# Kernel optimization log

Hardware: AMD Instinct MI355X
Metric: run time of the kernel (lower is better)

The kernel has to match this reference:

```python
import jax, jax.numpy as jnp
import numpy as np

# Config matching init_kwargs: dim=256, input_resolution=(64,64), num_heads=8,
# stride=2, dynamic_factor=2, window_size=8, Attention_Group=2, postype='rel', k=None
DIM, H, W = 256, 64, 64
HEADS, HG, STRIDE, WS, FACTOR = 8, 2, 2, 8, 2.0
GC = DIM // HG                 # channels per attention group (offset net width)
HC = DIM // HEADS              # per-head channels
RH, RW = H // STRIDE, W // STRIDE
WH, WW = H // WS, W // WS
B = 2
MLP_HID = 4 * DIM
EPS = 1e-5


def _grid_sample(img, grid):
    # img: (N, C, H, W); grid: (N, Hg, Wg, 2) with (row, col) in [-1, 1].
    # Bilinear, align_corners=True, zero padding (matches F.grid_sample).
    N, C, Hi, Wi = img.shape
    rows = (grid[..., 0] + 1.0) * 0.5 * (Hi - 1)
    cols = (grid[..., 1] + 1.0) * 0.5 * (Wi - 1)
    r0f = jnp.floor(rows); c0f = jnp.floor(cols)
    wr = rows - r0f; wc = cols - c0f
    r0 = r0f.astype(jnp.int32); c0 = c0f.astype(jnp.int32)

    def gather(ri, ci):
        valid = ((ri >= 0) & (ri < Hi) & (ci >= 0) & (ci < Wi)).astype(img.dtype)
        rc = jnp.clip(ri, 0, Hi - 1); cc = jnp.clip(ci, 0, Wi - 1)
        vals = jax.vmap(lambda im, r, c: im[:, r, c])(img, rc, cc)  # (N, C, Hg, Wg)
        return vals * valid[:, None]

    return (gather(r0, c0) * ((1 - wr) * (1 - wc))[:, None]
            + gather(r0, c0 + 1) * ((1 - wr) * wc)[:, None]
            + gather(r0 + 1, c0) * (wr * (1 - wc))[:, None]
            + gather(r0 + 1, c0 + 1) * (wr * wc)[:, None])


def _ln2d(z, g, b):
    mu = jnp.mean(z, axis=1, keepdims=True)
    var = jnp.var(z, axis=1, keepdims=True)
    return (z - mu) * jax.lax.rsqrt(var + EPS) * g[None, :, None, None] + b[None, :, None, None]


def _conv1x1(z, w, b=None):
    out = jnp.einsum('oc,bchw->bohw', w, z)
    return out if b is None else out + b[None, :, None, None]


def _forward(x, ln1_g, ln1_b, q_w, q_b, k_w, k_b, v_w, v_b,
             off1_w, off2_w, off3_w, bn_g, bn_b, bn_m, bn_v, off4_w,
             posembed, proj_w, proj_b, ln2_g, ln2_b,
             mlp_w1, mlp_b1, mlp_w2, mlp_b2):
    Bx, C = x.shape[0], x.shape[1]
    R, NW, WT = RH * RW, WH * WW, WS * WS
    scale = C ** -0.5  # original uses dim**-0.5 (not head_dim) as default qk scale

    xa = _ln2d(x, ln1_g, ln1_b)
    q = _conv1x1(xa, q_w, q_b)

    # ---- per-group offset prediction: 3 depthwise strided convs -> BN -> GELU -> 1x1 ----
    qg = q.reshape(Bx * HG, GC, H, W)

    def dw(z, w):
        return jax.lax.conv_general_dilated(z, w, (2, 2), ((1, 1), (1, 1)),
                feature_group_count=GC, dimension_numbers=('NCHW', 'OIHW', 'NCHW'))

    o = dw(dw(dw(qg, off1_w), off2_w), off3_w)  # (B*HG, GC, WH, WW)
    o = (o - bn_m[None, :, None, None]) * jax.lax.rsqrt(bn_v + EPS)[None, :, None, None]
    o = o * bn_g[None, :, None, None] + bn_b[None, :, None, None]
    o = jax.nn.gelu(o, approximate=False)
    off = jnp.einsum('oc,bchw->bohw', off4_w, o)               # (B*HG, 2R, WH, WW)
    off = off.reshape(Bx * HG, 2, R, NW).transpose(0, 3, 2, 1)  # (B*HG, NW, R, 2)
    ranges = jnp.array([1.0 / H, 1.0 / W], dtype=x.dtype)
    off = jnp.tanh(off) * ranges * FACTOR

    # ---- reference points normalized to [-1, 1] (align_corners=True convention) ----
    ref_r = (jnp.arange(RH, dtype=x.dtype) * STRIDE) / (H - 1) * 2.0 - 1.0
    ref_c = (jnp.arange(RW, dtype=x.dtype) * STRIDE) / (W - 1) * 2.0 - 1.0
    ref = jnp.stack(jnp.meshgrid(ref_r, ref_c, indexing='ij'), axis=-1).reshape(R, 2)
    grid = off + ref[None, None]                                # (B*HG, NW, R, 2)

    # ---- deformable gather of values at predicted sample locations ----
    value = xa.reshape(Bx * HG, GC, H, W)
    samp = _grid_sample(value, grid).reshape(Bx, C, NW, R)

    kk = _conv1x1(samp, k_w, k_b).reshape(Bx * HEADS, HC, NW, R).transpose(0, 2, 1, 3)
    vv = _conv1x1(samp, v_w, v_b).reshape(Bx * HEADS, HC, NW, R).transpose(0, 2, 1, 3)

    # ---- windowed queries ----
    wq = q.reshape(Bx * HEADS, HC, H, W).transpose(0, 2, 3, 1)
    wq = wq.reshape(Bx * HEADS, WH, WS, WW, WS, HC).transpose(0, 1, 3, 2, 4, 5)
    wq = wq.reshape(Bx * HEADS, NW, WT, HC) * scale

    attn = jnp.einsum('nwqc,nwcr->nwqr', wq, kk)                # (B*h, NW, WT, R)

    # ---- relative position bias: query pixel vs. (stride-spaced) reference point ----
    rel_y = (jnp.arange(RH) * STRIDE)[None, :] - jnp.arange(H)[:, None] + (H - 1)  # (H, RH)
    rel_x = (jnp.arange(RW) * STRIDE)[None, :] - jnp.arange(W)[:, None] + (W - 1)  # (W, RW)
    t = posembed[:, rel_y, :]                                   # (h, H, RH, 2W-1)
    bias = t[:, :, :, rel_x]                                    # (h, H, RH, W, RW)
    bias = bias.transpose(0, 1, 3, 2, 4).reshape(HEADS, H, W, R)
    bias = bias.reshape(HEADS, WH, WS, WW, WS, R).transpose(0, 1, 3, 2, 4, 5)
    bias = bias.reshape(HEADS, NW, WT, R)

    attn = attn.reshape(Bx, HEADS, NW, WT, R) + bias[None]
    attn = jax.nn.softmax(attn, axis=-1).reshape(Bx * HEADS, NW, WT, R)
    out = jnp.einsum('nwqr,nwcr->nwqc', attn, vv)               # (B*h, NW, WT, HC)
    out = out.reshape(Bx * HEADS, WH, WW, WS, WS, HC).transpose(0, 1, 3, 2, 4, 5)
    out = out.reshape(Bx, HEADS, H, W, HC).transpose(0, 1, 4, 2, 3).reshape(Bx, C, H, W)
    out = _conv1x1(out, proj_w, proj_b)

    x = x + out
    xm = _ln2d(x, ln2_g, ln2_b)
    hdn = jax.nn.gelu(_conv1x1(xm, mlp_w1, mlp_b1), approximate=False)
    return x + _conv1x1(hdn, mlp_w2, mlp_b2)


def setup_inputs() -> dict:
    key = jax.random.key(0)
    ks = jax.random.split(key, 16)
    f32 = jnp.float32

    def n(k, shape, std=0.02):
        return jax.random.normal(k, shape, dtype=f32) * std

    R = RH * RW
    return {
        'x': jax.random.normal(ks[0], (B, DIM, H, W), dtype=f32),
        'ln1_g': jnp.ones((DIM,), f32), 'ln1_b': jnp.zeros((DIM,), f32),
        'q_w': n(ks[1], (DIM, DIM)), 'q_b': jnp.zeros((DIM,), f32),
        'k_w': n(ks[2], (DIM, DIM)), 'k_b': jnp.zeros((DIM,), f32),
        'v_w': n(ks[3], (DIM, DIM)), 'v_b': jnp.zeros((DIM,), f32),
        'off1_w': n(ks[4], (GC, 1, 3, 3)),
        'off2_w': n(ks[5], (GC, 1, 3, 3)),
        'off3_w': n(ks[6], (GC, 1, 3, 3)),
        'bn_g': jnp.ones((GC,), f32), 'bn_b': jnp.zeros((GC,), f32),
        'bn_m': jnp.zeros((GC,), f32), 'bn_v': jnp.ones((GC,), f32),
        'off4_w': n(ks[7], (2 * R, GC)),
        'posembed': n(ks[8], (HEADS, 2 * H - 1, 2 * W - 1), std=0.01),
        'proj_w': n(ks[9], (DIM, DIM)), 'proj_b': jnp.zeros((DIM,), f32),
        'ln2_g': jnp.ones((DIM,), f32), 'ln2_b': jnp.zeros((DIM,), f32),
        'mlp_w1': n(ks[10], (MLP_HID, DIM)), 'mlp_b1': jnp.zeros((MLP_HID,), f32),
        'mlp_w2': n(ks[11], (DIM, MLP_HID)), 'mlp_b2': jnp.zeros((DIM,), f32),
    }


def reference(x, ln1_g, ln1_b, q_w, q_b, k_w, k_b, v_w, v_b,
              off1_w, off2_w, off3_w, bn_g, bn_b, bn_m, bn_v, off4_w,
              posembed, proj_w, proj_b, ln2_g, ln2_b,
              mlp_w1, mlp_b1, mlp_w2, mlp_b2):
    return _forward(x, ln1_g, ln1_b, q_w, q_b, k_w, k_b, v_w, v_b,
                    off1_w, off2_w, off3_w, bn_g, bn_b, bn_m, bn_v, off4_w,
                    posembed, proj_w, proj_b, ln2_g, ln2_b,
                    mlp_w1, mlp_b1, mlp_w2, mlp_b2)
```

## Files before the change

kernel.cpp:

```cpp
#include <hip/hip_runtime.h>
#include <hip/hip_bf16.h>
#include <math.h>


typedef __hip_bfloat16 bf16;
typedef __bf16 bf16x8 __attribute__((ext_vector_type(8)));
typedef float f32x4 __attribute__((ext_vector_type(4)));
typedef unsigned int u32x4 __attribute__((ext_vector_type(4)));

union U16x8 { uint4 u4; u32x4 v4; unsigned short us[8]; };
union FU { float f; unsigned int u; };

__device__ __forceinline__ float cvt(float x) { return x; }
__device__ __forceinline__ float cvt(bf16 x) { return __bfloat162float(x); }
__device__ __forceinline__ float b2f(unsigned short u) {
  union { float f; unsigned int v; } x; x.v = ((unsigned int)u) << 16; return x.f;
}
__device__ __forceinline__ float hi2f(unsigned int u) {
  FU x; x.u = u & 0xffff0000u; return x.f;
}
__device__ __forceinline__ float lo2f(unsigned int u) {
  FU x; x.u = u << 16; return x.f;
}
__device__ __forceinline__ unsigned short f2b(float f) {
  bf16 h = __float2bfloat16(f);
  return *reinterpret_cast<unsigned short*>(&h);
}
__device__ __forceinline__ float gelu_f(float x) {
  return 0.5f * x * (1.0f + erff(x * 0.7071067811865475f));
}
__device__ __forceinline__ void stout(float* p, float v) { *p = v; }
__device__ __forceinline__ void stout(bf16* p, float v) { *p = __float2bfloat16(v); }

__global__ __launch_bounds__(256) void setup_kernel(
    const float* __restrict__ x, const float* __restrict__ g,
    const float* __restrict__ bta,
    const float* __restrict__ q_w, const float* __restrict__ q_b,
    const float* __restrict__ k_w, const float* __restrict__ v_w,
    const float* __restrict__ pjw, const float* __restrict__ w1,
    const float* __restrict__ w2, const float* __restrict__ off4w,
    bf16* __restrict__ out, float* __restrict__ xnhwc,
    unsigned short* __restrict__ wqkv, float* __restrict__ bqkv,
    unsigned short* __restrict__ wproj, unsigned short* __restrict__ wmlp1,
    unsigned short* __restrict__ wmlp2, unsigned short* __restrict__ woff4i)
{
  __shared__ float s1[8][32], s2[8][32];
  __shared__ unsigned short tb[32][264];
  int bid = blockIdx.x;
  int t = threadIdx.x;
  if (bid < 256) {
    int pos = t & 31, cs = t >> 5;
    int p = bid * 32 + pos;
    int bb = p >> 12, hw = p & 4095;
    const float* xp = x + (size_t)bb * 256 * 4096 + hw;
    float vloc[32];
    float sum = 0.f, ss = 0.f;
#pragma unroll
    for (int i = 0; i < 32; ++i) {
      float v = xp[(size_t)(cs * 32 + i) * 4096];
      vloc[i] = v; sum += v; ss += v * v;
    }
    s1[cs][pos] = sum; s2[cs][pos] = ss;
    {
      float* xo = xnhwc + (size_t)p * 256 + cs * 32;
#pragma unroll
      for (int qd = 0; qd < 8; ++qd)
        *(float4*)(xo + qd * 4) = make_float4(vloc[qd*4], vloc[qd*4+1],
                                              vloc[qd*4+2], vloc[qd*4+3]);
    }
    __syncthreads();
    if (cs == 0) {
      float S = 0.f, Q = 0.f;
#pragma unroll
      for (int i = 0; i < 8; ++i) { S += s1[i][pos]; Q += s2[i][pos]; }
      float mu = S * (1.f / 256.f);
      float var = Q * (1.f / 256.f) - mu * mu;
      s1[0][pos] = mu;
      s2[0][pos] = rsqrtf(var + 1e-5f);
    }
    __syncthreads();
    float mu = s1[0][pos], rs = s2[0][pos];
#pragma unroll
    for (int i = 0; i < 32; ++i) {
      int c = cs * 32 + i;
      tb[pos][c] = f2b((vloc[i] - mu) * rs * g[c] + bta[c]);
    }
    __syncthreads();
    int px = t >> 3, grp = t & 7;
    bf16* op = out + ((size_t)bid * 32 + px) * 256 + grp * 32;
#pragma unroll
    for (int q = 0; q < 4; ++q)
      *(uint4*)(op + q * 8) = *(const uint4*)&tb[px][grp * 32 + q * 8];
  } else {
    int idx = (bid - 256) * 256 + t;
    const int S0 = 768 * 256;
    const int S1 = S0 + 768;
    const int S2 = S1 + 256 * 256;
    const int S3 = S2 + 1024 * 256;
    const int S4 = S3 + 256 * 1024;
    const int S5 = S4 + 2048 * 128;
    if (idx < S0) {
      int n = idx >> 8, c = idx & 255;
      float v;
      if (n < 256)       v = q_w[n * 256 + c];
      else if (n < 512)  v = k_w[(n - 256) * 256 + c];
      else               v = v_w[(n - 512) * 256 + c];
      wqkv[idx] = f2b(v);
    } else if (idx < S1) {
      int n = idx - S0;
      bqkv[n] = (n < 256) ? q_b[n] : 0.f;
    } else if (idx < S2) {
      wproj[idx - S1] = f2b(pjw[idx - S1]);
    } else if (idx < S3) {
      wmlp1[idx - S2] = f2b(w1[idx - S2]);
    } else if (idx < S4) {
      wmlp2[idx - S3] = f2b(w2[idx - S3]);
    } else if (idx < S5) {
      int kk = idx - S4;
      int n = kk >> 7, c = kk & 127;
      woff4i[kk] = f2b(off4w[((size_t)((n & 1) * 1024 + (n >> 1))) * 128 + c]);
    }
  }
}

__global__ __launch_bounds__(256) void ln2_kernel(
    const bf16* __restrict__ xin, const float* __restrict__ g,
    const float* __restrict__ bta, bf16* __restrict__ out)
{
  __shared__ float sa[8][32], sb[8][32];
  __shared__ float mu_s[32], rs_s[32];
  int t = threadIdx.x;
  int px = t >> 3, grp = t & 7;
  size_t p = (size_t)blockIdx.x * 32 + px;
  const bf16* xp = xin + p * 256 + grp * 32;
  float v[32]; float sum = 0.f, ss = 0.f;
#pragma unroll
  for (int q = 0; q < 4; ++q) {
    U16x8 u; u.u4 = *(const uint4*)(xp + q * 8);
#pragma unroll
    for (int j = 0; j < 8; ++j) {
      float f = b2f(u.us[j]); v[q * 8 + j] = f; sum += f; ss += f * f;
    }
  }
  sa[grp][px] = sum; sb[grp][px] = ss;
  __syncthreads();
  if (t < 32) {
    float S = 0.f, Q = 0.f;
#pragma unroll
    for (int i = 0; i < 8; ++i) { S += sa[i][t]; Q += sb[i][t]; }
    float mu = S * (1.f / 256.f);
    mu_s[t] = mu;
    rs_s[t] = rsqrtf(Q * (1.f / 256.f) - mu * mu + 1e-5f);
  }
  __syncthreads();
  float mu = mu_s[px], rs = rs_s[px];
  bf16* op = out + p * 256 + grp * 32;
#pragma unroll
  for (int q = 0; q < 4; ++q) {
    U16x8 o;
#pragma unroll
    for (int j = 0; j < 8; ++j) {
      int c = grp * 32 + q * 8 + j;
      o.us[j] = f2b((v[q * 8 + j] - mu) * rs * g[c] + bta[c]);
    }
    *(uint4*)(op + q * 8) = o.u4;
  }
}

template<int OUTM, int RESM, int ACT, int BM, int BN>
__global__ __launch_bounds__(256) void mgemm_kernel(
    const bf16* __restrict__ A, const unsigned short* __restrict__ Bw,
    const float* __restrict__ bias, const void* __restrict__ res,
    void* __restrict__ out, int N, int K, int lda, int ldb)
{
  constexpr int MT = BM / 32;
  constexpr int WNT = BN / 32;
  constexpr int AB_BYTES = (BM + BN) * 72 * 2;
  constexpr int T_LD = BM + 5;
  constexpr int T_BYTES = 64 * T_LD * 4;
  constexpr int SH_BYTES = (OUTM == 1 && T_BYTES > AB_BYTES) ? T_BYTES : AB_BYTES;
  __shared__ __attribute__((aligned(16))) char shraw[SH_BYTES];
  auto As = reinterpret_cast<unsigned short(*)[72]>(shraw);
  auto Bs = reinterpret_cast<unsigned short(*)[72]>(shraw + BM * 72 * 2);
  float (*T)[T_LD] = reinterpret_cast<float(*)[T_LD]>(shraw);

  int t = threadIdx.x;
  int m0 = blockIdx.y * BM, n0 = blockIdx.x * BN;
  int lane = t & 63, w = t >> 6;
  int l15 = lane & 15, quad = lane >> 4;
  int wm = (w >> 1) * (BM / 2), wn = (w & 1) * (BN / 2);
  f32x4 acc[MT][WNT];
#pragma unroll
  for (int mt = 0; mt < MT; ++mt)
#pragma unroll
    for (int nt = 0; nt < WNT; ++nt) acc[mt][nt] = (f32x4){0.f, 0.f, 0.f, 0.f};

  for (int k0 = 0; k0 < K; k0 += 64) {
#pragma unroll
    for (int i = 0; i < MT; ++i) {
      int idx = t + i * 256;
      int m = idx >> 3, oc = (idx & 7) * 8;
      *(uint4*)&As[m][oc] = *(const uint4*)(A + (size_t)(m0 + m) * lda + k0 + oc);
    }
#pragma unroll
    for (int i = 0; i < WNT; ++i) {
      int idx = t + i * 256;
      int n = idx >> 3, oc = (idx & 7) * 8;
      *(uint4*)&Bs[n][oc] = *(const uint4*)(Bw + (size_t)(n0 + n) * ldb + k0 + oc);
    }
    __syncthreads();
#pragma unroll
    for (int ks = 0; ks < 2; ++ks) {
      bf16x8 af[MT], bfr[WNT];
#pragma unroll
      for (int mt = 0; mt < MT; ++mt)
        af[mt] = __builtin_bit_cast(bf16x8,
            *(const uint4*)&As[wm + mt * 16 + l15][ks * 32 + quad * 8]);
#pragma unroll
      for (int nt = 0; nt < WNT; ++nt)
        bfr[nt] = __builtin_bit_cast(bf16x8,
            *(const uint4*)&Bs[wn + nt * 16 + l15][ks * 32 + quad * 8]);
#pragma unroll
      for (int mt = 0; mt < MT; ++mt)
#pragma unroll
        for (int nt = 0; nt < WNT; ++nt)
          acc[mt][nt] = __builtin_amdgcn_mfma_f32_16x16x32_bf16(
              af[mt], bfr[nt], acc[mt][nt], 0, 0, 0);
    }
    __syncthreads();
  }
  float bv[WNT];
#pragma unroll
  for (int nt = 0; nt < WNT; ++nt)
    bv[nt] = bias ? bias[n0 + wn + nt * 16 + l15] : 0.f;
#pragma unroll
  for (int mt = 0; mt < MT; ++mt) {
#pragma unroll
    for (int nt = 0; nt < WNT; ++nt) {
#pragma unroll
      for (int reg = 0; reg < 4; ++reg) {
        int m = m0 + wm + mt * 16 + quad * 4 + reg;
        int n = n0 + wn + nt * 16 + l15;
        float v = acc[mt][nt][reg] + bv[nt];
        if constexpr (ACT == 1) v = gelu_f(v);
        if constexpr (RESM == 1)
          v += ((const float*)res)[(size_t)m * N + n];
        if constexpr (RESM == 2)
          v += b2f(((const unsigned short*)res)[(size_t)m * N + n]);
        if constexpr (OUTM == 0)
          ((unsigned short*)out)[(size_t)m * N + n] = f2b(v);
        if constexpr (OUTM == 1)
          T[(n - n0)][(m - m0)] = v;
        if constexpr (OUTM == 4)
          ((unsigned short*)out)[((size_t)(n >> 8) * 8192 + m) * 256 + (n & 255)] = f2b(v);
        if constexpr (OUTM == 5) {
          float val = tanhf(v) * (2.0f / 64.0f);
          int r = n >> 1, coord = n & 1;
          int rc = coord ? (r & 31) : (r >> 5);
          float ref = rc * (4.0f / 63.0f) - 1.0f;
          float pix = (val + ref + 1.0f) * 31.5f;
          float other = __shfl_xor(pix, 1, 64);
          if (coord == 0) {
            float rowp = pix, colp = other;
            float r0f = floorf(rowp), c0f = floorf(colp);
            float wr = rowp - r0f, wc = colp - c0f;
            int r0 = (int)r0f, c0 = (int)c0f;
            bool rv0 = ((unsigned)r0 < 64u), rv1 = ((unsigned)(r0 + 1) < 64u);
            bool cv0 = ((unsigned)c0 < 64u), cv1 = ((unsigned)(c0 + 1) < 64u);
            float4 w4;
            w4.x = (rv0 && cv0) ? (1.f - wr) * (1.f - wc) : 0.f;
            w4.y = (rv0 && cv1) ? (1.f - wr) * wc : 0.f;
            w4.z = (rv1 && cv0) ? wr * (1.f - wc) : 0.f;
            w4.w = (rv1 && cv1) ? wr * wc : 0.f;
            ((int*)out)[(size_t)m * 1024 + r] = r0 * 64 + c0;
            *(float4*)((float*)res + ((size_t)m * 1024 + r) * 4) = w4;
          }
        }
      }
    }
  }
  if constexpr (OUTM == 1) {
    __syncthreads();
    constexpr int SEGS = BM / 32;
    int units = 64 * SEGS;
    if (t < units) {
      int nl = t / SEGS, seg = t % SEGS;
      int bI = m0 >> 12, hw0 = m0 & 4095;
      float* op = (float*)out + ((size_t)bI * 256 + n0 + nl) * 4096 + hw0 + seg * 32;
#pragma unroll
      for (int k = 0; k < 32; ++k) op[k] = T[nl][seg * 32 + k];
    }
  }
}

template<typename TI, typename TO, int IC>
__global__ __launch_bounds__(256) void dwconv_kernel(
    const TI* __restrict__ in, const float* __restrict__ wgt,
    TO* __restrict__ out, int Hi, int Wi, int Ho, int Wo, int fuse,
    const float* __restrict__ bg_, const float* __restrict__ bb_,
    const float* __restrict__ bm_, const float* __restrict__ bv_)
{
  int idx = blockIdx.x * 256 + threadIdx.x;
  int c = idx & 127;
  int pp = idx >> 7;
  int ow = pp % Wo, oh = (pp / Wo) % Ho, bgi = pp / (Wo * Ho);
  const TI* ip;
  if constexpr (IC == 256)
    ip = in + ((size_t)(bgi >> 1) * 4096) * 256 + (bgi & 1) * 128 + c;
  else
    ip = in + ((size_t)bgi * Hi * Wi) * 128 + c;
  float acc = 0.f;
#pragma unroll
  for (int ky = 0; ky < 3; ++ky) {
    int ih = oh * 2 - 1 + ky;
    if ((unsigned)ih >= (unsigned)Hi) continue;
#pragma unroll
    for (int kx = 0; kx < 3; ++kx) {
      int iw = ow * 2 - 1 + kx;
      if ((unsigned)iw >= (unsigned)Wi) continue;
      acc += wgt[c * 9 + ky * 3 + kx] * cvt(ip[(size_t)(ih * Wi + iw) * IC]);
    }
  }
  if (fuse) {
    acc = (acc - bm_[c]) * rsqrtf(bv_[c] + 1e-5f) * bg_[c] + bb_[c];
    acc = gelu_f(acc);
  }
  stout(out + idx, acc);
}

__global__ __launch_bounds__(256) void gatherkv_kernel(
    const unsigned short* __restrict__ Kimg, const unsigned short* __restrict__ Vimg,
    const int* __restrict__ goff, const float* __restrict__ gwt,
    unsigned short* __restrict__ Ks, unsigned short* __restrict__ Vs)
{
  int t = threadIdx.x;
  int pos = blockIdx.x * 8 + (t >> 5);
  int oct = t & 31;
  int r = pos & 1023;
  int nw = (pos >> 10) & 63;
  int b = pos >> 16;
  int ch0 = oct * 8;
  int g = oct >> 4;

  size_t cbase = ((size_t)(b * 2 + g) * 64 + nw) * 1024 + r;
  int base = goff[cbase];
  f32x4 wv = *(const f32x4*)(gwt + cbase * 4);
  int o00 = min(max(base, 0), 4095);
  int o01 = min(max(base + 1, 0), 4095);
  int o10 = min(max(base + 64, 0), 4095);
  int o11 = min(max(base + 65, 0), 4095);
  size_t pb = ((size_t)b * 4096) * 256 + ch0;
  uint4 kc[4], vc[4];
  kc[0] = *(const uint4*)(Kimg + pb + (size_t)o00 * 256);
  kc[1] = *(const uint4*)(Kimg + pb + (size_t)o01 * 256);
  kc[2] = *(const uint4*)(Kimg + pb + (size_t)o10 * 256);
  kc[3] = *(const uint4*)(Kimg + pb + (size_t)o11 * 256);
  vc[0] = *(const uint4*)(Vimg + pb + (size_t)o00 * 256);
  vc[1] = *(const uint4*)(Vimg + pb + (size_t)o01 * 256);
  vc[2] = *(const uint4*)(Vimg + pb + (size_t)o10 * 256);
  vc[3] = *(const uint4*)(Vimg + pb + (size_t)o11 * 256);

  float aK[8] = {0.f,0.f,0.f,0.f,0.f,0.f,0.f,0.f};
  float aV[8] = {0.f,0.f,0.f,0.f,0.f,0.f,0.f,0.f};
#pragma unroll
  for (int c4 = 0; c4 < 4; ++c4) {
    U16x8 ku, vu; ku.u4 = kc[c4]; vu.u4 = vc[c4];
    float wvv = wv[c4];
#pragma unroll
    for (int j = 0; j < 8; ++j) {
      aK[j] += wvv * b2f(ku.us[j]);
      aV[j] += wvv * b2f(vu.us[j]);
    }
  }
  U16x8 ok, ov;
#pragma unroll
  for (int j = 0; j < 8; ++j) { ok.us[j] = f2b(aK[j]); ov.us[j] = f2b(aV[j]); }
  int head = oct >> 2, chh = (oct & 3) * 8;
  size_t obase = (((size_t)(b * 8 + head) * 64 + nw) * 1024 + r) * 32 + chh;
  __builtin_nontemporal_store(ok.v4, (u32x4*)(Ks + obase));
  __builtin_nontemporal_store(ov.v4, (u32x4*)(Vs + obase));
}

__global__ __launch_bounds__(256) void attn2_kernel(
    const bf16* __restrict__ qbuf, const unsigned short* __restrict__ Ks,
    const unsigned short* __restrict__ Vs, const float* __restrict__ vbv,
    const float* __restrict__ pe, bf16* __restrict__ aout)
{
  __shared__ unsigned short vs[2][32][72];
  __shared__ unsigned short PsQs[64][72];
  __shared__ unsigned short pesb[70][72];

  const float LOG2E = 1.4426950408889634f;
  int blk = blockIdx.x;
  int b = blk & 1, head = (blk >> 1) & 7, nw = blk >> 4;
  int wh = nw >> 3, ww = nw & 7;
  int t = threadIdx.x;
  int lane = t & 63, w = t >> 6;
  int l15 = lane & 15, quad = lane >> 4;
  int qc0 = head * 32;
  int vr = t >> 2, vseg = t & 3;

  size_t kvbase = ((size_t)(b * 8 + head) * 64 + nw) * 32768;
  const unsigned short* Kb = Ks + kvbase;
  const unsigned short* Vb = Vs + kvbase;

  {
    int qt = t >> 2, oct = t & 3;
    int h = wh * 8 + (qt >> 3), wcol = ww * 8 + (qt & 7);
    const bf16* src = qbuf + ((size_t)b * 4096 + h * 64 + wcol) * 256 + qc0 + oct * 8;
    U16x8 u; u.u4 = *(const uint4*)src;
    U16x8 o;
#pragma unroll
    for (int j = 0; j < 8; ++j) o.us[j] = f2b(b2f(u.us[j]) * (0.0625f * LOG2E));
    *(uint4*)&PsQs[qt][oct * 8] = o.u4;
  }
  int ry0 = 56 - wh * 8, rx0 = 56 - ww * 8;
  for (int i = t; i < 70 * 70; i += 256) {
    int yy = i / 70, xx = i % 70;
    pesb[yy][xx] = f2b(pe[(size_t)head * 16129 + (ry0 + yy) * 127 + rx0 + xx] * LOG2E);
  }
  {
    U16x8 vu; vu.u4 = *(const uint4*)(Vb + (size_t)t * 8);
#pragma unroll
    for (int j = 0; j < 8; ++j) {
      int row = vseg * 8 + j;
      vs[0][row][vr ^ (((row >> 3) & 3) * 8)] = vu.us[j];
    }
  }
  uint4 kf[4];
#pragma unroll
  for (int nt = 0; nt < 4; ++nt)
    kf[nt] = *(const uint4*)(Kb + (size_t)(nt * 16 + l15) * 32 + quad * 8);
  __syncthreads();

  bf16x8 aQ = __builtin_bit_cast(bf16x8, *(const uint4*)&PsQs[w * 16 + l15][quad * 8]);
  float l[4] = {0.f, 0.f, 0.f, 0.f};
  f32x4 oacc[2];
  oacc[0] = (f32x4){0.f, 0.f, 0.f, 0.f};
  oacc[1] = (f32x4){0.f, 0.f, 0.f, 0.f};

  int rowbase = 7 - (w * 2 + (quad >> 1));
  int Cb = 2 * l15 + 7 - (quad & 1) * 4;

  uint4 vcn = make_uint4(0u, 0u, 0u, 0u);
  uint4 kfn[4];
  for (int c = 0; c < 16; ++c) {
    int cur = c & 1;
    if (c) {
      U16x8 vu; vu.u4 = vcn;
#pragma unroll
      for (int j = 0; j < 8; ++j) {
        int row = vseg * 8 + j;
        vs[cur][row][vr ^ (((row >> 3) & 3) * 8)] = vu.us[j];
      }
      __syncthreads();
    }
    if (c < 15) {
      size_t nb = (size_t)(c * 64 + 64) * 32;
      vcn = *(const uint4*)(Vb + nb + (size_t)t * 8);
#pragma unroll
      for (int nt = 0; nt < 4; ++nt)
        kfn[nt] = *(const uint4*)(Kb + nb + (size_t)(nt * 16 + l15) * 32 + quad * 8);
    }

    f32x4 s[4];
    __builtin_amdgcn_s_setprio(1);
#pragma unroll
    for (int nt = 0; nt < 4; ++nt) {
      bf16x8 bK = __builtin_bit_cast(bf16x8, kf[nt]);
      f32x4 z = (f32x4){0.f, 0.f, 0.f, 0.f};
      s[nt] = __builtin_amdgcn_mfma_f32_16x16x32_bf16(aQ, bK, z, 0, 0, 0);
    }
    __builtin_amdgcn_s_setprio(0);
#pragma unroll
    for (int nt = 0; nt < 4; ++nt) {
      int row = rowbase + 4 * c + 2 * (nt >> 1);
      int C = Cb + (nt & 1) * 32;
      const unsigned int* pr = (const unsigned int*)&pesb[row][0];
      unsigned int pa = pr[(C - 3) >> 1];
      unsigned int pbm = pr[(C - 1) >> 1];
      s[nt][0] += hi2f(pbm);
      s[nt][1] += lo2f(pbm);
      s[nt][2] += hi2f(pa);
      s[nt][3] += lo2f(pa);
    }
#pragma unroll
    for (int reg = 0; reg < 4; ++reg) {
      float ps = 0.f;
#pragma unroll
      for (int nt = 0; nt < 4; ++nt) {
        float p = exp2f(s[nt][reg]);
        PsQs[w * 16 + quad * 4 + reg][nt * 16 + l15] = f2b(p);
        ps += p;
      }
      l[reg] += ps;
    }
    __builtin_amdgcn_s_setprio(1);
#pragma unroll
    for (int kst = 0; kst < 2; ++kst) {
      uint4 up = *(const uint4*)&PsQs[w * 16 + l15][kst * 32 + quad * 8];
      bf16x8 pA = __builtin_bit_cast(bf16x8, up);
#pragma unroll
      for (int nt2 = 0; nt2 < 2; ++nt2) {
        int row = nt2 * 16 + l15;
        int cbase = (kst * 32 + quad * 8) ^ (((row >> 3) & 3) * 8);
        uint4 uv = *(const uint4*)&vs[cur][row][cbase];
        bf16x8 vB = __builtin_bit_cast(bf16x8, uv);
        oacc[nt2] = __builtin_amdgcn_mfma_f32_16x16x32_bf16(pA, vB, oacc[nt2], 0, 0, 0);
      }
    }
    __builtin_amdgcn_s_setprio(0);
    if (c < 15) {
#pragma unroll
      for (int nt = 0; nt < 4; ++nt) kf[nt] = kfn[nt];
    }
  }
#pragma unroll
  for (int reg = 0; reg < 4; ++reg) {
    l[reg] += __shfl_xor(l[reg], 1, 64);
    l[reg] += __shfl_xor(l[reg], 2, 64);
    l[reg] += __shfl_xor(l[reg], 4, 64);
    l[reg] += __shfl_xor(l[reg], 8, 64);
  }
#pragma unroll
  for (int nt2 = 0; nt2 < 2; ++nt2) {
    float vbias = vbv[qc0 + nt2 * 16 + l15];
#pragma unroll
    for (int reg = 0; reg < 4; ++reg) {
      int q = w * 16 + quad * 4 + reg;
      size_t p = (size_t)b * 4096 + (wh * 8 + (q >> 3)) * 64 + ww * 8 + (q & 7);
      aout[p * 256 + qc0 + nt2 * 16 + l15] =
          __float2bfloat16(oacc[nt2][reg] / l[reg] + vbias);
    }
  }
}

extern "C" void kernel_launch(void* const* d_in, const int* in_sizes, int n_in,
                              void* d_out, int out_size, void* d_ws, size_t ws_size,
                              hipStream_t stream) {
  (void)in_sizes; (void)n_in; (void)out_size; (void)ws_size;
  const float* x     = (const float*)d_in[0];
  const float* ln1g  = (const float*)d_in[1];
  const float* ln1b  = (const float*)d_in[2];
  const float* q_w   = (const float*)d_in[3];
  const float* q_b   = (const float*)d_in[4];
  const float* k_w   = (const float*)d_in[5];
  const float* k_b   = (const float*)d_in[6];
  const float* v_w   = (const float*)d_in[7];
  const float* v_b   = (const float*)d_in[8];
  const float* off1w = (const float*)d_in[9];
  const float* off2w = (const float*)d_in[10];
  const float* off3w = (const float*)d_in[11];
  const float* bng   = (const float*)d_in[12];
  const float* bnb   = (const float*)d_in[13];
  const float* bnm   = (const float*)d_in[14];
  const float* bnv   = (const float*)d_in[15];
  const float* off4w = (const float*)d_in[16];
  const float* pe    = (const float*)d_in[17];
  const float* pjw   = (const float*)d_in[18];
  const float* pjb   = (const float*)d_in[19];
  const float* ln2g  = (const float*)d_in[20];
  const float* ln2b  = (const float*)d_in[21];
  const float* w1    = (const float*)d_in[22];
  const float* b1    = (const float*)d_in[23];
  const float* w2    = (const float*)d_in[24];
  const float* b2    = (const float*)d_in[25];
  (void)k_b;
  float* outp = (float*)d_out;

  char* W = (char*)d_ws;
  bf16*  xa    = (bf16*) (W + 0);
  float* dw1   = (float*)(W + 8388608);
  float* dw2   = (float*)(W + 10485760);
  bf16*  dw3b  = (bf16*) (W + 11010048);
  bf16*  qkv   = (bf16*) (W + 13238272);
  bf16*  qb    = qkv;
  bf16*  Kimg  = qkv + 2097152;
  bf16*  Vimg  = qkv + 2 * 2097152;
  bf16*  x2    = (bf16*) (W + 34209792);
  float* xnhwc = (float*)(W + 38404096);
  unsigned short* wqkv   = (unsigned short*)(W + 46792704);
  float*          bqkv   = (float*)         (W + 47448064);
  unsigned short* wproj  = (unsigned short*)(W + 47453184);
  unsigned short* wmlp1  = (unsigned short*)(W + 47584256);
  unsigned short* wmlp2  = (unsigned short*)(W + 48108544);
  unsigned short* woff4i = (unsigned short*)(W + 48632832);
  int*   goff  = (int*)  (W + 49157120);
  float* gwt   = (float*)(W + 50205696);
  unsigned short* Ksmp = (unsigned short*)(W + 54525952);
  unsigned short* Vsmp = (unsigned short*)(W + 121634816);
  bf16*  aout = xa;
  bf16*  xm   = xa;
  bf16*  hdn  = Kimg;

  setup_kernel<<<4356, 256, 0, stream>>>(
      x, ln1g, ln1b, q_w, q_b, k_w, v_w, pjw, w1, w2, off4w,
      xa, xnhwc, wqkv, bqkv, wproj, wmlp1, wmlp2, woff4i);
  mgemm_kernel<4, 0, 0, 128, 128><<<dim3(6, 64), 256, 0, stream>>>(
      xa, wqkv, bqkv, nullptr, qkv, 768, 256, 256, 256);
  dwconv_kernel<bf16, float, 256><<<2048, 256, 0, stream>>>(
      qb, off1w, dw1, 64, 64, 32, 32, 0, nullptr, nullptr, nullptr, nullptr);
  dwconv_kernel<float, float, 128><<<512, 256, 0, stream>>>(
      dw1, off2w, dw2, 32, 32, 16, 16, 0, nullptr, nullptr, nullptr, nullptr);
  dwconv_kernel<float, bf16, 128><<<128, 256, 0, stream>>>(
      dw2, off3w, dw3b, 16, 16, 8, 8, 1, bng, bnb, bnm, bnv);
  mgemm_kernel<5, 0, 0, 64, 64><<<dim3(32, 4), 256, 0, stream>>>(
      dw3b, woff4i, nullptr, (const void*)gwt, goff, 2048, 128, 128, 128);
  gatherkv_kernel<<<16384, 256, 0, stream>>>(
      (const unsigned short*)Kimg, (const unsigned short*)Vimg,
      goff, gwt, Ksmp, Vsmp);
  attn2_kernel<<<1024, 256, 0, stream>>>(
      qb, Ksmp, Vsmp, v_b, pe, aout);
  mgemm_kernel<0, 1, 0, 64, 128><<<dim3(2, 128), 256, 0, stream>>>(
      aout, wproj, pjb, (const void*)xnhwc, x2, 256, 256, 256, 256);
  ln2_kernel<<<256, 256, 0, stream>>>(x2, ln2g, ln2b, xm);
  mgemm_kernel<0, 0, 1, 128, 128><<<dim3(8, 64), 256, 0, stream>>>(
      xm, wmlp1, b1, nullptr, hdn, 1024, 256, 256, 256);
  mgemm_kernel<1, 2, 0, 64, 64><<<dim3(4, 128), 256, 0, stream>>>(
      hdn, wmlp2, b2, (const void*)x2, outp, 256, 1024, 1024, 1024);
}
```

Baseline: 278.9 us.

## Fuse bilinear K/V gather into attention kernel and retune GEMM tiles

Removes the separate gather kernel that wrote sampled K/V to large global buffers. The attention kernel now gathers and bilinearly combines K/V for each 64-key chunk directly into double-buffered shared memory, overlapping the next chunk's loads with the current chunk's MFMAs. This eliminates a large global write and re-read of intermediate K/V. The price is more per-block load latency and register pressure in attention. The tile widths of several GEMM launches are also halved to get more blocks.

```diff
diff --git a/kernel.cpp b/kernel.cpp
--- a/kernel.cpp
+++ b/kernel.cpp
@@ -328,64 +328,13 @@
   stout(out + idx, acc);
 }
 
-__global__ __launch_bounds__(256) void gatherkv_kernel(
-    const unsigned short* __restrict__ Kimg, const unsigned short* __restrict__ Vimg,
-    const int* __restrict__ goff, const float* __restrict__ gwt,
-    unsigned short* __restrict__ Ks, unsigned short* __restrict__ Vs)
-{
-  int t = threadIdx.x;
-  int pos = blockIdx.x * 8 + (t >> 5);
-  int oct = t & 31;
-  int r = pos & 1023;
-  int nw = (pos >> 10) & 63;
-  int b = pos >> 16;
-  int ch0 = oct * 8;
-  int g = oct >> 4;
-
-  size_t cbase = ((size_t)(b * 2 + g) * 64 + nw) * 1024 + r;
-  int base = goff[cbase];
-  f32x4 wv = *(const f32x4*)(gwt + cbase * 4);
-  int o00 = min(max(base, 0), 4095);
-  int o01 = min(max(base + 1, 0), 4095);
-  int o10 = min(max(base + 64, 0), 4095);
-  int o11 = min(max(base + 65, 0), 4095);
-  size_t pb = ((size_t)b * 4096) * 256 + ch0;
-  uint4 kc[4], vc[4];
-  kc[0] = *(const uint4*)(Kimg + pb + (size_t)o00 * 256);
-  kc[1] = *(const uint4*)(Kimg + pb + (size_t)o01 * 256);
-  kc[2] = *(const uint4*)(Kimg + pb + (size_t)o10 * 256);
-  kc[3] = *(const uint4*)(Kimg + pb + (size_t)o11 * 256);
-  vc[0] = *(const uint4*)(Vimg + pb + (size_t)o00 * 256);
-  vc[1] = *(const uint4*)(Vimg + pb + (size_t)o01 * 256);
-  vc[2] = *(const uint4*)(Vimg + pb + (size_t)o10 * 256);
-  vc[3] = *(const uint4*)(Vimg + pb + (size_t)o11 * 256);
-
-  float aK[8] = {0.f,0.f,0.f,0.f,0.f,0.f,0.f,0.f};
-  float aV[8] = {0.f,0.f,0.f,0.f,0.f,0.f,0.f,0.f};
-#pragma unroll
-  for (int c4 = 0; c4 < 4; ++c4) {
-    U16x8 ku, vu; ku.u4 = kc[c4]; vu.u4 = vc[c4];
-    float wvv = wv[c4];
-#pragma unroll
-    for (int j = 0; j < 8; ++j) {
-      aK[j] += wvv * b2f(ku.us[j]);
-      aV[j] += wvv * b2f(vu.us[j]);
-    }
-  }
-  U16x8 ok, ov;
-#pragma unroll
-  for (int j = 0; j < 8; ++j) { ok.us[j] = f2b(aK[j]); ov.us[j] = f2b(aV[j]); }
-  int head = oct >> 2, chh = (oct & 3) * 8;
-  size_t obase = (((size_t)(b * 8 + head) * 64 + nw) * 1024 + r) * 32 + chh;
-  __builtin_nontemporal_store(ok.v4, (u32x4*)(Ks + obase));
-  __builtin_nontemporal_store(ov.v4, (u32x4*)(Vs + obase));
-}
-
-__global__ __launch_bounds__(256) void attn2_kernel(
-    const bf16* __restrict__ qbuf, const unsigned short* __restrict__ Ks,
-    const unsigned short* __restrict__ Vs, const float* __restrict__ vbv,
+__global__ __launch_bounds__(256) void attn4_kernel(
+    const bf16* __restrict__ qbuf, const unsigned short* __restrict__ Kimg,
+    const unsigned short* __restrict__ Vimg, const int* __restrict__ goff,
+    const float* __restrict__ gwt, const float* __restrict__ vbv,
     const float* __restrict__ pe, bf16* __restrict__ aout)
 {
+  __shared__ unsigned short ks[2][64][40];
   __shared__ unsigned short vs[2][32][72];
   __shared__ unsigned short PsQs[64][72];
   __shared__ unsigned short pesb[70][72];
@@ -398,11 +347,54 @@
   int lane = t & 63, w = t >> 6;
   int l15 = lane & 15, quad = lane >> 4;
   int qc0 = head * 32;
-  int vr = t >> 2, vseg = t & 3;
-
-  size_t kvbase = ((size_t)(b * 8 + head) * 64 + nw) * 32768;
-  const unsigned short* Kb = Ks + kvbase;
-  const unsigned short* Vb = Vs + kvbase;
+  int g = head >> 2;
+  int gr_r = t >> 2, gr_seg = t & 3;
+  int choff = qc0 + gr_seg * 8;
+  size_t cb0 = ((size_t)(b * 2 + g) * 64 + nw) * 1024 + gr_r;
+  size_t pbK = (size_t)b * 4096 * 256 + choff;
+
+  uint4 kc[4], vc[4];
+  f32x4 wv;
+  auto gather = [&](int rc0) {
+    size_t cbase = cb0 + rc0;
+    int base = goff[cbase];
+    wv = *(const f32x4*)(gwt + cbase * 4);
+    int o00 = min(max(base, 0), 4095);
+    int o01 = min(max(base + 1, 0), 4095);
+    int o10 = min(max(base + 64, 0), 4095);
+    int o11 = min(max(base + 65, 0), 4095);
+    kc[0] = *(const uint4*)(Kimg + pbK + (size_t)o00 * 256);
+    kc[1] = *(const uint4*)(Kimg + pbK + (size_t)o01 * 256);
+    kc[2] = *(const uint4*)(Kimg + pbK + (size_t)o10 * 256);
+    kc[3] = *(const uint4*)(Kimg + pbK + (size_t)o11 * 256);
+    vc[0] = *(const uint4*)(Vimg + pbK + (size_t)o00 * 256);
+    vc[1] = *(const uint4*)(Vimg + pbK + (size_t)o01 * 256);
+    vc[2] = *(const uint4*)(Vimg + pbK + (size_t)o10 * 256);
+    vc[3] = *(const uint4*)(Vimg + pbK + (size_t)o11 * 256);
+  };
+  auto combine = [&](int buf) {
+    float aK[8] = {0.f,0.f,0.f,0.f,0.f,0.f,0.f,0.f};
+    float aV[8] = {0.f,0.f,0.f,0.f,0.f,0.f,0.f,0.f};
+#pragma unroll
+    for (int c4 = 0; c4 < 4; ++c4) {
+      U16x8 ku, vu; ku.u4 = kc[c4]; vu.u4 = vc[c4];
+      float wvv = wv[c4];
+#pragma unroll
+      for (int j = 0; j < 8; ++j) {
+        aK[j] += wvv * b2f(ku.us[j]);
+        aV[j] += wvv * b2f(vu.us[j]);
+      }
+    }
+    U16x8 ok;
+#pragma unroll
+    for (int j = 0; j < 8; ++j) ok.us[j] = f2b(aK[j]);
+    *(uint4*)&ks[buf][gr_r][gr_seg * 8] = ok.u4;
+#pragma unroll
+    for (int j = 0; j < 8; ++j) {
+      int row = gr_seg * 8 + j;
+      vs[buf][row][gr_r ^ (((row >> 3) & 3) * 8)] = f2b(aV[j]);
+    }
+  };
 
   {
     int qt = t >> 2, oct = t & 3;
@@ -419,18 +411,8 @@
     int yy = i / 70, xx = i % 70;
     pesb[yy][xx] = f2b(pe[(size_t)head * 16129 + (ry0 + yy) * 127 + rx0 + xx] * LOG2E);
   }
-  {
-    U16x8 vu; vu.u4 = *(const uint4*)(Vb + (size_t)t * 8);
-#pragma unroll
-    for (int j = 0; j < 8; ++j) {
-      int row = vseg * 8 + j;
-      vs[0][row][vr ^ (((row >> 3) & 3) * 8)] = vu.us[j];
-    }
-  }
-  uint4 kf[4];
-#pragma unroll
-  for (int nt = 0; nt < 4; ++nt)
-    kf[nt] = *(const uint4*)(Kb + (size_t)(nt * 16 + l15) * 32 + quad * 8);
+  gather(0);
+  combine(0);
   __syncthreads();
 
   bf16x8 aQ = __builtin_bit_cast(bf16x8, *(const uint4*)&PsQs[w * 16 + l15][quad * 8]);
@@ -442,32 +424,17 @@
   int rowbase = 7 - (w * 2 + (quad >> 1));
   int Cb = 2 * l15 + 7 - (quad & 1) * 4;
 
-  uint4 vcn = make_uint4(0u, 0u, 0u, 0u);
-  uint4 kfn[4];
   for (int c = 0; c < 16; ++c) {
     int cur = c & 1;
-    if (c) {
-      U16x8 vu; vu.u4 = vcn;
-#pragma unroll
-      for (int j = 0; j < 8; ++j) {
-        int row = vseg * 8 + j;
-        vs[cur][row][vr ^ (((row >> 3) & 3) * 8)] = vu.us[j];
-      }
-      __syncthreads();
-    }
-    if (c < 15) {
-      size_t nb = (size_t)(c * 64 + 64) * 32;
-      vcn = *(const uint4*)(Vb + nb + (size_t)t * 8);
-#pragma unroll
-      for (int nt = 0; nt < 4; ++nt)
-        kfn[nt] = *(const uint4*)(Kb + nb + (size_t)(nt * 16 + l15) * 32 + quad * 8);
-    }
+    if (c) __syncthreads();
+    if (c < 15) gather(c * 64 + 64);
 
     f32x4 s[4];
     __builtin_amdgcn_s_setprio(1);
 #pragma unroll
     for (int nt = 0; nt < 4; ++nt) {
-      bf16x8 bK = __builtin_bit_cast(bf16x8, kf[nt]);
+      uint4 u = *(const uint4*)&ks[cur][nt * 16 + l15][quad * 8];
+      bf16x8 bK = __builtin_bit_cast(bf16x8, u);
       f32x4 z = (f32x4){0.f, 0.f, 0.f, 0.f};
       s[nt] = __builtin_amdgcn_mfma_f32_16x16x32_bf16(aQ, bK, z, 0, 0, 0);
     }
@@ -510,10 +477,7 @@
       }
     }
     __builtin_amdgcn_s_setprio(0);
-    if (c < 15) {
-#pragma unroll
-      for (int nt = 0; nt < 4; ++nt) kf[nt] = kfn[nt];
-    }
+    if (c < 15) combine(cur ^ 1);
   }
 #pragma unroll
   for (int reg = 0; reg < 4; ++reg) {
@@ -587,8 +551,6 @@
   unsigned short* woff4i = (unsigned short*)(W + 48632832);
   int*   goff  = (int*)  (W + 49157120);
   float* gwt   = (float*)(W + 50205696);
-  unsigned short* Ksmp = (unsigned short*)(W + 54525952);
-  unsigned short* Vsmp = (unsigned short*)(W + 121634816);
   bf16*  aout = xa;
   bf16*  xm   = xa;
   bf16*  hdn  = Kimg;
@@ -596,7 +558,7 @@
   setup_kernel<<<4356, 256, 0, stream>>>(
       x, ln1g, ln1b, q_w, q_b, k_w, v_w, pjw, w1, w2, off4w,
       xa, xnhwc, wqkv, bqkv, wproj, wmlp1, wmlp2, woff4i);
-  mgemm_kernel<4, 0, 0, 128, 128><<<dim3(6, 64), 256, 0, stream>>>(
+  mgemm_kernel<4, 0, 0, 128, 64><<<dim3(12, 64), 256, 0, stream>>>(
       xa, wqkv, bqkv, nullptr, qkv, 768, 256, 256, 256);
   dwconv_kernel<bf16, float, 256><<<2048, 256, 0, stream>>>(
       qb, off1w, dw1, 64, 64, 32, 32, 0, nullptr, nullptr, nullptr, nullptr);
@@ -606,15 +568,13 @@
       dw2, off3w, dw3b, 16, 16, 8, 8, 1, bng, bnb, bnm, bnv);
   mgemm_kernel<5, 0, 0, 64, 64><<<dim3(32, 4), 256, 0, stream>>>(
       dw3b, woff4i, nullptr, (const void*)gwt, goff, 2048, 128, 128, 128);
-  gatherkv_kernel<<<16384, 256, 0, stream>>>(
-      (const unsigned short*)Kimg, (const unsigned short*)Vimg,
-      goff, gwt, Ksmp, Vsmp);
-  attn2_kernel<<<1024, 256, 0, stream>>>(
-      qb, Ksmp, Vsmp, v_b, pe, aout);
-  mgemm_kernel<0, 1, 0, 64, 128><<<dim3(2, 128), 256, 0, stream>>>(
+  attn4_kernel<<<1024, 256, 0, stream>>>(
+      qb, (const unsigned short*)Kimg, (const unsigned short*)Vimg,
+      goff, gwt, v_b, pe, aout);
+  mgemm_kernel<0, 1, 0, 64, 64><<<dim3(4, 128), 256, 0, stream>>>(
       aout, wproj, pjb, (const void*)xnhwc, x2, 256, 256, 256, 256);
   ln2_kernel<<<256, 256, 0, stream>>>(x2, ln2g, ln2b, xm);
-  mgemm_kernel<0, 0, 1, 128, 128><<<dim3(8, 64), 256, 0, stream>>>(
+  mgemm_kernel<0, 0, 1, 128, 64><<<dim3(16, 64), 256, 0, stream>>>(
       xm, wmlp1, b1, nullptr, hdn, 1024, 256, 256, 256);
   mgemm_kernel<1, 2, 0, 64, 64><<<dim3(4, 128), 256, 0, stream>>>(
       hdn, wmlp2, b2, (const void*)x2, outp, 256, 1024, 1024, 1024);
```

Result: no change. 277.0 us (-0.7%).
